# Performance work log

Measured on AMD Instinct MI355X. Metric: run time of the kernel, lower is better.

## Reference

```python
import jax, jax.numpy as jnp
import numpy as np

B, C_IN, C_OUT, H, W = 4, 256, 256, 64, 64
KH = KW = 3
STRIDE = 1
PAD = 1
DIL = 1


def setup_inputs() -> dict:
    key = jax.random.key(0)
    k1, k2, k3, k4 = jax.random.split(key, 4)
    x = jax.random.normal(k1, (B, C_IN, H, W), dtype=jnp.float32)
    # torchvision layout: 2*dg*KH*KW channels, (y, x) pair per kernel tap
    offset = jax.random.normal(k2, (B, 2 * KH * KW, H, W), dtype=jnp.float32)
    fan_in = C_IN * KH * KW
    weight = jax.random.normal(k3, (C_OUT, C_IN, KH, KW), dtype=jnp.float32) / np.sqrt(fan_in)
    bias = jax.random.normal(k4, (C_OUT,), dtype=jnp.float32) * 0.01
    return {"x": x, "offset": offset, "weight": weight, "bias": bias}


def _gather_bilinear_corner(x_flat, yi, xi, h, w):
    # x_flat: [B, C, H*W]; yi/xi: [B, KK, Ho, Wo] int32
    valid = ((yi >= 0) & (yi < h) & (xi >= 0) & (xi < w)).astype(x_flat.dtype)
    idx = jnp.clip(yi, 0, h - 1) * w + jnp.clip(xi, 0, w - 1)
    b = idx.shape[0]
    g = jnp.take_along_axis(x_flat, idx.reshape(b, 1, -1), axis=2)
    return g.reshape(b, x_flat.shape[1], *yi.shape[1:]), valid


def deform_conv2d(x, offset, weight, bias):
    b, c, h, w = x.shape
    o = weight.shape[0]
    kk = KH * KW
    ho = (h + 2 * PAD - DIL * (KH - 1) - 1) // STRIDE + 1
    wo = (w + 2 * PAD - DIL * (KW - 1) - 1) // STRIDE + 1

    ky = (jnp.arange(kk, dtype=jnp.float32) // KW) * DIL  # [KK]
    kx = (jnp.arange(kk, dtype=jnp.float32) % KW) * DIL
    hs = jnp.arange(ho, dtype=jnp.float32) * STRIDE - PAD   # [Ho]
    ws = jnp.arange(wo, dtype=jnp.float32) * STRIDE - PAD   # [Wo]

    off = offset.reshape(b, kk, 2, ho, wo)
    py = hs[None, None, :, None] + ky[None, :, None, None] + off[:, :, 0]  # [B,KK,Ho,Wo]
    px = ws[None, None, None, :] + kx[None, :, None, None] + off[:, :, 1]

    y0 = jnp.floor(py)
    x0 = jnp.floor(px)
    wy1 = py - y0  # fractional parts, differentiable w.r.t. offsets
    wx1 = px - x0
    wy0 = 1.0 - wy1
    wx0 = 1.0 - wx1
    y0i = y0.astype(jnp.int32)
    x0i = x0.astype(jnp.int32)

    x_flat = x.reshape(b, c, h * w)
    corners = [
        (y0i,     x0i,     wy0 * wx0),
        (y0i,     x0i + 1, wy0 * wx1),
        (y0i + 1, x0i,     wy1 * wx0),
        (y0i + 1, x0i + 1, wy1 * wx1),
    ]
    sampled = jnp.zeros((b, c, kk, ho, wo), dtype=x.dtype)
    for yi, xi, wgt in corners:
        g, valid = _gather_bilinear_corner(x_flat, yi, xi, h, w)
        sampled = sampled + g * (wgt * valid)[:, None]

    out = jnp.einsum('bckhw,ock->bohw', sampled, weight.reshape(o, c, kk))
    return out + bias[None, :, None, None]


def reference(x, offset, weight, bias):
    return deform_conv2d(x, offset, weight, bias)
```

## Files before the change

kernel.cpp:

```cpp
#include <hip/hip_runtime.h>

typedef __bf16 bf16;
typedef __bf16 bf16x4 __attribute__((ext_vector_type(4)));
typedef __bf16 bf16x8 __attribute__((ext_vector_type(8)));
typedef float  f32x4  __attribute__((ext_vector_type(4)));

#define CIN   256
#define KK    9
#define KDIM  2304
#define KITERS 72
#define PXW   32
#define SROW  264

__device__ __forceinline__ float sread(float f) {
    return __builtin_bit_cast(float,
        __builtin_amdgcn_readfirstlane(__builtin_bit_cast(int, f)));
}
__device__ __forceinline__ int sreadi(int v) {
    return __builtin_amdgcn_readfirstlane(v);
}

__global__ __launch_bounds__(256) void prep_k(const float* __restrict__ x,
                                              const float* __restrict__ w,
                                              bf16* __restrict__ xt,
                                              bf16* __restrict__ wq) {
    int bid = blockIdx.x;
    int tid = threadIdx.x;
    if (bid < 1024) {
        __shared__ bf16 tile[64][72];
        int pt = bid & 63, ct = (bid >> 6) & 3, b = bid >> 8;
        int lane = tid & 63, row = tid >> 6;
        const float* src = x + ((size_t)(b * 256 + ct * 64)) * 4096 + pt * 64;
        #pragma unroll
        for (int cc = row; cc < 64; cc += 4)
            tile[lane][cc] = (bf16)src[(size_t)cc * 4096 + lane];
        __syncthreads();
        bf16* dst = xt + ((size_t)(b * 4096 + pt * 64)) * 256 + ct * 64;
        int p = tid >> 3, j = tid & 7;
        #pragma unroll
        for (int pp = p; pp < 64; pp += 32)
            *reinterpret_cast<bf16x8*>(dst + (size_t)pp * 256 + j * 8) =
                *reinterpret_cast<const bf16x8*>(&tile[pp][j * 8]);
    } else {
        int idx  = (bid - 1024) * 256 + tid;
        int j    = idx & 7;
        int lane = (idx >> 3) & 63;
        int rest = idx >> 9;
        int kt   = rest % KITERS;
        int m    = rest / KITERS;
        int l16  = lane & 15;
        int quad = lane >> 4;
        int o    = m * 16 + l16;
        int k    = kt * 32 + quad * 8 + j;
        int tap  = k >> 8;
        int cc   = k & 255;
        wq[idx] = (bf16)w[(size_t)o * KDIM + cc * KK + tap];
    }
}

__global__ __launch_bounds__(512, 4) void deform_gemm_k(
    const bf16*  __restrict__ xt,
    const float* __restrict__ off,
    const bf16*  __restrict__ wq,
    const float* __restrict__ bias,
    float*       __restrict__ out) {

    __shared__ bf16 S[PXW][SROW];

    int tid   = threadIdx.x;
    int wavei = sreadi(tid >> 6);
    int lane  = tid & 63;
    int quad  = lane >> 4;
    int l16   = lane & 15;

    int bid   = blockIdx.x;
    int pb    = ((bid & 7) << 6) | (bid >> 3);
    int pix0  = pb * PXW;
    int b     = pix0 >> 12;
    int pimgb = pix0 & 4095;
    int obase = b * 73728;
    unsigned base = (unsigned)b * 1048576u + (unsigned)(lane * 4);

    f32x4 acc[2][2];
    #pragma unroll
    for (int mt = 0; mt < 2; ++mt)
        #pragma unroll
        for (int nt = 0; nt < 2; ++nt)
            acc[mt][nt] = (f32x4){0.f, 0.f, 0.f, 0.f};

    for (int tap = 0; tap < KK; ++tap) {
        int ty = tap / 3 - 1;
        int tx = tap % 3 - 1;

        int u[4][4];
        float wt[4][4];
        #pragma unroll
        for (int i = 0; i < 4; ++i) {
            int pimg = pimgb + wavei * 4 + i;
            float oy = off[obase + pimg + (2 * tap) * 4096];
            float ox = off[obase + pimg + (2 * tap + 1) * 4096];
            float py = (float)((pimg >> 6) + ty) + oy;
            float px = (float)((pimg & 63) + tx) + ox;
            float fy = floorf(py), fx = floorf(px);
            int   y0 = (int)fy,    x0 = (int)fx;
            float wy1 = py - fy, wx1 = px - fx;
            float wy0 = 1.f - wy1, wx0 = 1.f - wx1;
            wy0 = ((unsigned)y0       < 64u) ? wy0 : 0.f;
            wy1 = ((unsigned)(y0 + 1) < 64u) ? wy1 : 0.f;
            wx0 = ((unsigned)x0       < 64u) ? wx0 : 0.f;
            wx1 = ((unsigned)(x0 + 1) < 64u) ? wx1 : 0.f;
            int yc0 = min(max(y0, 0), 63),     yc1 = min(max(y0 + 1, 0), 63);
            int xc0 = min(max(x0, 0), 63),     xc1 = min(max(x0 + 1, 0), 63);
            u[i][0] = sreadi((yc0 * 64 + xc0) * 256);
            u[i][1] = sreadi((yc0 * 64 + xc1) * 256);
            u[i][2] = sreadi((yc1 * 64 + xc0) * 256);
            u[i][3] = sreadi((yc1 * 64 + xc1) * 256);
            wt[i][0] = sread(wy0 * wx0); wt[i][1] = sread(wy0 * wx1);
            wt[i][2] = sread(wy1 * wx0); wt[i][3] = sread(wy1 * wx1);
        }
        bf16x4 v[4][4];
        #pragma unroll
        for (int i = 0; i < 4; ++i)
            #pragma unroll
            for (int j = 0; j < 4; ++j)
                v[i][j] = *reinterpret_cast<const bf16x4*>(xt + base + (unsigned)u[i][j]);
        #pragma unroll
        for (int i = 0; i < 4; ++i) {
            float a0 = 0.f, a1 = 0.f, a2 = 0.f, a3 = 0.f;
            #pragma unroll
            for (int j = 0; j < 4; ++j) {
                float wgt = wt[i][j];
                a0 += wgt * (float)v[i][j][0];
                a1 += wgt * (float)v[i][j][1];
                a2 += wgt * (float)v[i][j][2];
                a3 += wgt * (float)v[i][j][3];
            }
            bf16x4 sv;
            sv[0] = (bf16)a0; sv[1] = (bf16)a1;
            sv[2] = (bf16)a2; sv[3] = (bf16)a3;
            *reinterpret_cast<bf16x4*>(&S[wavei * 4 + i][lane * 4]) = sv;
        }
        __syncthreads();

        const bf16* sp0 = &S[l16][quad * 8];
        const bf16* sp1 = &S[16 + l16][quad * 8];
        const bf16* ap0 = wq + ((size_t)((2 * wavei) * KITERS + tap * 8) * 64 + lane) * 8;
        const bf16* ap1 = ap0 + (size_t)KITERS * 64 * 8;
        #pragma unroll
        for (int kki = 0; kki < 8; ++kki) {
            bf16x8 b0 = *reinterpret_cast<const bf16x8*>(sp0 + kki * 32);
            bf16x8 b1 = *reinterpret_cast<const bf16x8*>(sp1 + kki * 32);
            bf16x8 a0 = *reinterpret_cast<const bf16x8*>(ap0 + (size_t)kki * 512);
            bf16x8 a1 = *reinterpret_cast<const bf16x8*>(ap1 + (size_t)kki * 512);
            acc[0][0] = __builtin_amdgcn_mfma_f32_16x16x32_bf16(a0, b0, acc[0][0], 0, 0, 0);
            acc[0][1] = __builtin_amdgcn_mfma_f32_16x16x32_bf16(a0, b1, acc[0][1], 0, 0, 0);
            acc[1][0] = __builtin_amdgcn_mfma_f32_16x16x32_bf16(a1, b0, acc[1][0], 0, 0, 0);
            acc[1][1] = __builtin_amdgcn_mfma_f32_16x16x32_bf16(a1, b1, acc[1][1], 0, 0, 0);
        }
        __syncthreads();
    }

    #pragma unroll
    for (int nt = 0; nt < 2; ++nt) {
        int pg   = pix0 + nt * 16 + l16;
        int bb   = pg >> 12;
        int pimg = pg & 4095;
        #pragma unroll
        for (int mt = 0; mt < 2; ++mt) {
            int m = (2 * wavei + mt) * 16 + quad * 4;
            float* op = out + ((size_t)(bb * 256 + m)) * 4096 + pimg;
            #pragma unroll
            for (int r = 0; r < 4; ++r)
                op[(size_t)r * 4096] = acc[mt][nt][r] + bias[m + r];
        }
    }
}

extern "C" void kernel_launch(void* const* d_in, const int* in_sizes, int n_in,
                              void* d_out, int out_size, void* d_ws, size_t ws_size,
                              hipStream_t stream) {
    const float* x    = (const float*)d_in[0];
    const float* off  = (const float*)d_in[1];
    const float* w    = (const float*)d_in[2];
    const float* bias = (const float*)d_in[3];
    float* out = (float*)d_out;

    bf16* wq = (bf16*)d_ws;
    bf16* xt = (bf16*)((char*)d_ws + (size_t)589824 * 2);

    prep_k<<<3328, 256, 0, stream>>>(x, w, xt, wq);
    deform_gemm_k<<<512, 512, 0, stream>>>(xt, off, wq, bias, out);
}
```

Measured before the change: 119.9 us.

## Widen pixel tile to 64 with 16 waves and XOR-swizzled LDS layout

Doubles the pixel tile per block to 64 and uses 1024 threads, so each of the 16 waves owns one 16-row output-channel slice across four 16-pixel column tiles. Each weight fragment loaded from global memory is now reused across four MFMAs instead of two, which halves total weight traffic. The padded LDS rows are replaced by an XOR swizzle meant to avoid bank conflicts. In exchange the grid shrinks to 256 blocks with 1024 threads each, which lowers occupancy and puts more threads behind each barrier.

```diff
diff --git a/kernel.cpp b/kernel.cpp
--- a/kernel.cpp
+++ b/kernel.cpp
@@ -9,8 +9,7 @@
 #define KK    9
 #define KDIM  2304
 #define KITERS 72
-#define PXW   32
-#define SROW  264
+#define PXW   64
 
 __device__ __forceinline__ float sread(float f) {
     return __builtin_bit_cast(float,
@@ -58,14 +57,14 @@
     }
 }
 
-__global__ __launch_bounds__(512, 4) void deform_gemm_k(
+__global__ __launch_bounds__(1024, 4) void deform_gemm_k(
     const bf16*  __restrict__ xt,
     const float* __restrict__ off,
     const bf16*  __restrict__ wq,
     const float* __restrict__ bias,
     float*       __restrict__ out) {
 
-    __shared__ bf16 S[PXW][SROW];
+    __shared__ bf16 S[PXW * 256];
 
     int tid   = threadIdx.x;
     int wavei = sreadi(tid >> 6);
@@ -74,19 +73,19 @@
     int l16   = lane & 15;
 
     int bid   = blockIdx.x;
-    int pb    = ((bid & 7) << 6) | (bid >> 3);
+    int pb    = ((bid & 7) << 5) | (bid >> 3);
     int pix0  = pb * PXW;
     int b     = pix0 >> 12;
     int pimgb = pix0 & 4095;
     int obase = b * 73728;
     unsigned base = (unsigned)b * 1048576u + (unsigned)(lane * 4);
 
-    f32x4 acc[2][2];
+    f32x4 acc[4];
     #pragma unroll
-    for (int mt = 0; mt < 2; ++mt)
-        #pragma unroll
-        for (int nt = 0; nt < 2; ++nt)
-            acc[mt][nt] = (f32x4){0.f, 0.f, 0.f, 0.f};
+    for (int nt = 0; nt < 4; ++nt)
+        acc[nt] = (f32x4){0.f, 0.f, 0.f, 0.f};
+
+    int q3 = lane & 7;
 
     for (int tap = 0; tap < KK; ++tap) {
         int ty = tap / 3 - 1;
@@ -138,41 +137,37 @@
             bf16x4 sv;
             sv[0] = (bf16)a0; sv[1] = (bf16)a1;
             sv[2] = (bf16)a2; sv[3] = (bf16)a3;
-            *reinterpret_cast<bf16x4*>(&S[wavei * 4 + i][lane * 4]) = sv;
+            int n   = wavei * 4 + i;
+            int gsw = (lane >> 1) ^ (n & 7);
+            *reinterpret_cast<bf16x4*>(&S[n * 256 + gsw * 8 + (lane & 1) * 4]) = sv;
         }
         __syncthreads();
 
-        const bf16* sp0 = &S[l16][quad * 8];
-        const bf16* sp1 = &S[16 + l16][quad * 8];
-        const bf16* ap0 = wq + ((size_t)((2 * wavei) * KITERS + tap * 8) * 64 + lane) * 8;
-        const bf16* ap1 = ap0 + (size_t)KITERS * 64 * 8;
+        const bf16* ap0 = wq + ((size_t)((wavei * KITERS + tap * 8) * 64 + lane)) * 8;
         #pragma unroll
         for (int kki = 0; kki < 8; ++kki) {
-            bf16x8 b0 = *reinterpret_cast<const bf16x8*>(sp0 + kki * 32);
-            bf16x8 b1 = *reinterpret_cast<const bf16x8*>(sp1 + kki * 32);
-            bf16x8 a0 = *reinterpret_cast<const bf16x8*>(ap0 + (size_t)kki * 512);
-            bf16x8 a1 = *reinterpret_cast<const bf16x8*>(ap1 + (size_t)kki * 512);
-            acc[0][0] = __builtin_amdgcn_mfma_f32_16x16x32_bf16(a0, b0, acc[0][0], 0, 0, 0);
-            acc[0][1] = __builtin_amdgcn_mfma_f32_16x16x32_bf16(a0, b1, acc[0][1], 0, 0, 0);
-            acc[1][0] = __builtin_amdgcn_mfma_f32_16x16x32_bf16(a1, b0, acc[1][0], 0, 0, 0);
-            acc[1][1] = __builtin_amdgcn_mfma_f32_16x16x32_bf16(a1, b1, acc[1][1], 0, 0, 0);
+            bf16x8 a = *reinterpret_cast<const bf16x8*>(ap0 + (size_t)kki * 512);
+            #pragma unroll
+            for (int nt = 0; nt < 4; ++nt) {
+                int row = nt * 16 + l16;
+                int g   = (kki * 4 + quad) ^ q3;
+                bf16x8 bb = *reinterpret_cast<const bf16x8*>(&S[row * 256 + g * 8]);
+                acc[nt] = __builtin_amdgcn_mfma_f32_16x16x32_bf16(a, bb, acc[nt], 0, 0, 0);
+            }
         }
         __syncthreads();
     }
 
     #pragma unroll
-    for (int nt = 0; nt < 2; ++nt) {
+    for (int nt = 0; nt < 4; ++nt) {
         int pg   = pix0 + nt * 16 + l16;
-        int bb   = pg >> 12;
+        int bb_  = pg >> 12;
         int pimg = pg & 4095;
+        int m    = wavei * 16 + quad * 4;
+        float* op = out + ((size_t)(bb_ * 256 + m)) * 4096 + pimg;
         #pragma unroll
-        for (int mt = 0; mt < 2; ++mt) {
-            int m = (2 * wavei + mt) * 16 + quad * 4;
-            float* op = out + ((size_t)(bb * 256 + m)) * 4096 + pimg;
-            #pragma unroll
-            for (int r = 0; r < 4; ++r)
-                op[(size_t)r * 4096] = acc[mt][nt][r] + bias[m + r];
-        }
+        for (int r = 0; r < 4; ++r)
+            op[(size_t)r * 4096] = acc[nt][r] + bias[m + r];
     }
 }
 
@@ -189,5 +184,5 @@
     bf16* xt = (bf16*)((char*)d_ws + (size_t)589824 * 2);
 
     prep_k<<<3328, 256, 0, stream>>>(x, w, xt, wq);
-    deform_gemm_k<<<512, 512, 0, stream>>>(xt, off, wq, bias, out);
+    deform_gemm_k<<<256, 1024, 0, stream>>>(xt, off, wq, bias, out);
 }
```

Result: no change. 121.2 us (+1.1%).

## Double-buffer sampled tile and overlap next-tap gather with current MFMA

Applied to the files above, without the earlier changes.

Splits the per-tap loop into a software pipeline. The bilinear gather for tap t+1 is interleaved with the MFMA GEMM for tap t through a double-buffered LDS tile, with sched_barriers forcing the interleave. This also removes one of the two __syncthreads per tap. The padded LDS rows are replaced by an XOR swizzle to avoid bank conflicts, which doubles LDS use and raises register pressure from holding the prefetched gathers and weight fragments.

```diff
diff --git a/kernel.cpp b/kernel.cpp
--- a/kernel.cpp
+++ b/kernel.cpp
@@ -10,7 +10,6 @@
 #define KDIM  2304
 #define KITERS 72
 #define PXW   32
-#define SROW  264
 
 __device__ __forceinline__ float sread(float f) {
     return __builtin_bit_cast(float,
@@ -65,7 +64,7 @@
     const float* __restrict__ bias,
     float*       __restrict__ out) {
 
-    __shared__ bf16 S[PXW][SROW];
+    __shared__ bf16 S[2][PXW * 256];
 
     int tid   = threadIdx.x;
     int wavei = sreadi(tid >> 6);
@@ -88,76 +87,133 @@
         for (int nt = 0; nt < 2; ++nt)
             acc[mt][nt] = (f32x4){0.f, 0.f, 0.f, 0.f};
 
-    for (int tap = 0; tap < KK; ++tap) {
-        int ty = tap / 3 - 1;
-        int tx = tap % 3 - 1;
-
-        int u[4][4];
-        float wt[4][4];
+    auto load_offs = [&](int tap, float* oy, float* ox) {
         #pragma unroll
         for (int i = 0; i < 4; ++i) {
             int pimg = pimgb + wavei * 4 + i;
-            float oy = off[obase + pimg + (2 * tap) * 4096];
-            float ox = off[obase + pimg + (2 * tap + 1) * 4096];
-            float py = (float)((pimg >> 6) + ty) + oy;
-            float px = (float)((pimg & 63) + tx) + ox;
-            float fy = floorf(py), fx = floorf(px);
-            int   y0 = (int)fy,    x0 = (int)fx;
-            float wy1 = py - fy, wx1 = px - fx;
-            float wy0 = 1.f - wy1, wx0 = 1.f - wx1;
-            wy0 = ((unsigned)y0       < 64u) ? wy0 : 0.f;
-            wy1 = ((unsigned)(y0 + 1) < 64u) ? wy1 : 0.f;
-            wx0 = ((unsigned)x0       < 64u) ? wx0 : 0.f;
-            wx1 = ((unsigned)(x0 + 1) < 64u) ? wx1 : 0.f;
-            int yc0 = min(max(y0, 0), 63),     yc1 = min(max(y0 + 1, 0), 63);
-            int xc0 = min(max(x0, 0), 63),     xc1 = min(max(x0 + 1, 0), 63);
-            u[i][0] = sreadi((yc0 * 64 + xc0) * 256);
-            u[i][1] = sreadi((yc0 * 64 + xc1) * 256);
-            u[i][2] = sreadi((yc1 * 64 + xc0) * 256);
-            u[i][3] = sreadi((yc1 * 64 + xc1) * 256);
-            wt[i][0] = sread(wy0 * wx0); wt[i][1] = sread(wy0 * wx1);
-            wt[i][2] = sread(wy1 * wx0); wt[i][3] = sread(wy1 * wx1);
-        }
-        bf16x4 v[4][4];
-        #pragma unroll
-        for (int i = 0; i < 4; ++i)
+            oy[i] = off[obase + pimg + (2 * tap) * 4096];
+            ox[i] = off[obase + pimg + (2 * tap + 1) * 4096];
+        }
+    };
+
+    auto gather_px = [&](int tap, int i, float oy, float ox,
+                         bf16x4* vv, float* wv) {
+        int pimg = pimgb + wavei * 4 + i;
+        float py = (float)((pimg >> 6) + tap / 3 - 1) + oy;
+        float px = (float)((pimg & 63) + tap % 3 - 1) + ox;
+        float fy = floorf(py), fx = floorf(px);
+        int   y0 = (int)fy,    x0 = (int)fx;
+        float wy1 = py - fy, wx1 = px - fx;
+        float wy0 = 1.f - wy1, wx0 = 1.f - wx1;
+        wy0 = ((unsigned)y0       < 64u) ? wy0 : 0.f;
+        wy1 = ((unsigned)(y0 + 1) < 64u) ? wy1 : 0.f;
+        wx0 = ((unsigned)x0       < 64u) ? wx0 : 0.f;
+        wx1 = ((unsigned)(x0 + 1) < 64u) ? wx1 : 0.f;
+        int yc0 = min(max(y0, 0), 63), yc1 = min(max(y0 + 1, 0), 63);
+        int xc0 = min(max(x0, 0), 63), xc1 = min(max(x0 + 1, 0), 63);
+        int u0 = sreadi((yc0 * 64 + xc0) * 256);
+        int u1 = sreadi((yc0 * 64 + xc1) * 256);
+        int u2 = sreadi((yc1 * 64 + xc0) * 256);
+        int u3 = sreadi((yc1 * 64 + xc1) * 256);
+        wv[0] = sread(wy0 * wx0); wv[1] = sread(wy0 * wx1);
+        wv[2] = sread(wy1 * wx0); wv[3] = sread(wy1 * wx1);
+        vv[0] = *reinterpret_cast<const bf16x4*>(xt + base + (unsigned)u0);
+        vv[1] = *reinterpret_cast<const bf16x4*>(xt + base + (unsigned)u1);
+        vv[2] = *reinterpret_cast<const bf16x4*>(xt + base + (unsigned)u2);
+        vv[3] = *reinterpret_cast<const bf16x4*>(xt + base + (unsigned)u3);
+    };
+
+    auto blend_px = [&](bf16* Sw, int i, const bf16x4* vv, const float* wv) {
+        float a0 = 0.f, a1 = 0.f, a2 = 0.f, a3 = 0.f;
+        #pragma unroll
+        for (int j = 0; j < 4; ++j) {
+            float wgt = wv[j];
+            a0 += wgt * (float)vv[j][0];
+            a1 += wgt * (float)vv[j][1];
+            a2 += wgt * (float)vv[j][2];
+            a3 += wgt * (float)vv[j][3];
+        }
+        bf16x4 sv;
+        sv[0] = (bf16)a0; sv[1] = (bf16)a1;
+        sv[2] = (bf16)a2; sv[3] = (bf16)a3;
+        int n  = wavei * 4 + i;
+        int gw = lane >> 1;
+        int gs = (gw & 24) | ((gw ^ (n & 7)) & 7);
+        *reinterpret_cast<bf16x4*>(Sw + n * 256 + gs * 8 + (lane & 1) * 4) = sv;
+    };
+
+    auto load_a = [&](int tap, int h, bf16x8 a[2][4]) {
+        #pragma unroll
+        for (int mt = 0; mt < 2; ++mt)
             #pragma unroll
-            for (int j = 0; j < 4; ++j)
-                v[i][j] = *reinterpret_cast<const bf16x4*>(xt + base + (unsigned)u[i][j]);
-        #pragma unroll
-        for (int i = 0; i < 4; ++i) {
-            float a0 = 0.f, a1 = 0.f, a2 = 0.f, a3 = 0.f;
-            #pragma unroll
-            for (int j = 0; j < 4; ++j) {
-                float wgt = wt[i][j];
-                a0 += wgt * (float)v[i][j][0];
-                a1 += wgt * (float)v[i][j][1];
-                a2 += wgt * (float)v[i][j][2];
-                a3 += wgt * (float)v[i][j][3];
+            for (int kk = 0; kk < 4; ++kk) {
+                int kt = tap * 8 + h * 4 + kk;
+                a[mt][kk] = *reinterpret_cast<const bf16x8*>(
+                    wq + ((size_t)(((2 * wavei + mt) * KITERS + kt) * 64 + lane)) * 8);
             }
-            bf16x4 sv;
-            sv[0] = (bf16)a0; sv[1] = (bf16)a1;
-            sv[2] = (bf16)a2; sv[3] = (bf16)a3;
-            *reinterpret_cast<bf16x4*>(&S[wavei * 4 + i][lane * 4]) = sv;
-        }
+    };
+
+    auto gemm_half = [&](const bf16* Sr, int h, bf16x8 a[2][4]) {
+        #pragma unroll
+        for (int kk = 0; kk < 4; ++kk) {
+            int kki = h * 4 + kk;
+            int g   = kki * 4 + quad;
+            int gs  = (g & 24) | ((g ^ (l16 & 7)) & 7);
+            bf16x8 b0 = *reinterpret_cast<const bf16x8*>(Sr + l16 * 256 + gs * 8);
+            bf16x8 b1 = *reinterpret_cast<const bf16x8*>(Sr + (16 + l16) * 256 + gs * 8);
+            acc[0][0] = __builtin_amdgcn_mfma_f32_16x16x32_bf16(a[0][kk], b0, acc[0][0], 0, 0, 0);
+            acc[0][1] = __builtin_amdgcn_mfma_f32_16x16x32_bf16(a[0][kk], b1, acc[0][1], 0, 0, 0);
+            acc[1][0] = __builtin_amdgcn_mfma_f32_16x16x32_bf16(a[1][kk], b0, acc[1][0], 0, 0, 0);
+            acc[1][1] = __builtin_amdgcn_mfma_f32_16x16x32_bf16(a[1][kk], b1, acc[1][1], 0, 0, 0);
+        }
+    };
+
+    {
+        float oy[4], ox[4];
+        load_offs(0, oy, ox);
+        bf16x4 v[4][4]; float wv[4][4];
+        #pragma unroll
+        for (int i = 0; i < 4; ++i) gather_px(0, i, oy[i], ox[i], v[i], wv[i]);
+        #pragma unroll
+        for (int i = 0; i < 4; ++i) blend_px(&S[0][0], i, v[i], wv[i]);
+    }
+    __syncthreads();
+
+    for (int t = 0; t < 8; ++t) {
+        const bf16* Sr = &S[t & 1][0];
+        bf16*       Sw = &S[(t & 1) ^ 1][0];
+        float oy[4], ox[4];
+        load_offs(t + 1, oy, ox);
+
+        bf16x8 alo[2][4];
+        load_a(t, 0, alo);
+        __builtin_amdgcn_sched_barrier(0);
+        bf16x4 v[4][4]; float wv[4][4];
+        gather_px(t + 1, 0, oy[0], ox[0], v[0], wv[0]);
+        gather_px(t + 1, 1, oy[1], ox[1], v[1], wv[1]);
+        __builtin_amdgcn_sched_barrier(0);
+        gemm_half(Sr, 0, alo);
+
+        bf16x8 ahi[2][4];
+        load_a(t, 1, ahi);
+        __builtin_amdgcn_sched_barrier(0);
+        gather_px(t + 1, 2, oy[2], ox[2], v[2], wv[2]);
+        gather_px(t + 1, 3, oy[3], ox[3], v[3], wv[3]);
+        __builtin_amdgcn_sched_barrier(0);
+        gemm_half(Sr, 1, ahi);
+
+        #pragma unroll
+        for (int i = 0; i < 4; ++i) blend_px(Sw, i, v[i], wv[i]);
         __syncthreads();
-
-        const bf16* sp0 = &S[l16][quad * 8];
-        const bf16* sp1 = &S[16 + l16][quad * 8];
-        const bf16* ap0 = wq + ((size_t)((2 * wavei) * KITERS + tap * 8) * 64 + lane) * 8;
-        const bf16* ap1 = ap0 + (size_t)KITERS * 64 * 8;
-        #pragma unroll
-        for (int kki = 0; kki < 8; ++kki) {
-            bf16x8 b0 = *reinterpret_cast<const bf16x8*>(sp0 + kki * 32);
-            bf16x8 b1 = *reinterpret_cast<const bf16x8*>(sp1 + kki * 32);
-            bf16x8 a0 = *reinterpret_cast<const bf16x8*>(ap0 + (size_t)kki * 512);
-            bf16x8 a1 = *reinterpret_cast<const bf16x8*>(ap1 + (size_t)kki * 512);
-            acc[0][0] = __builtin_amdgcn_mfma_f32_16x16x32_bf16(a0, b0, acc[0][0], 0, 0, 0);
-            acc[0][1] = __builtin_amdgcn_mfma_f32_16x16x32_bf16(a0, b1, acc[0][1], 0, 0, 0);
-            acc[1][0] = __builtin_amdgcn_mfma_f32_16x16x32_bf16(a1, b0, acc[1][0], 0, 0, 0);
-            acc[1][1] = __builtin_amdgcn_mfma_f32_16x16x32_bf16(a1, b1, acc[1][1], 0, 0, 0);
-        }
-        __syncthreads();
+    }
+
+    {
+        const bf16* Sr = &S[0][0];
+        bf16x8 alo[2][4], ahi[2][4];
+        load_a(8, 0, alo);
+        load_a(8, 1, ahi);
+        gemm_half(Sr, 0, alo);
+        gemm_half(Sr, 1, ahi);
     }
 
     #pragma unroll
```

After: 119.3 us. No clear change (-0.6%).
